# Kernel tuning notes

Measured on AMD Instinct MI355X. Metric: run time of the kernel, lower is better.

## Reference

```python
import jax, jax.numpy as jnp
import numpy as np

B, N, M, K = 4, 32768, 32768, 16
HID, DIM, G = 64, 32, 4
GN_EPS = 1e-5


def _conv1x1(x, w, b):
    # x: [B,C,N,K], w: [O,C], b: [O]  (1x1 Conv2d)
    return jnp.einsum('oc,bcnk->bonk', w, x) + b[None, :, None, None]


def _group_norm(x, w, b, groups):
    Bb, C, Nn, Kk = x.shape
    xg = x.reshape(Bb, groups, C // groups, Nn, Kk)
    mu = xg.mean(axis=(2, 3, 4), keepdims=True)
    var = xg.var(axis=(2, 3, 4), keepdims=True)
    xg = (xg - mu) * jax.lax.rsqrt(var + GN_EPS)
    x = xg.reshape(Bb, C, Nn, Kk)
    return x * w[None, :, None, None] + b[None, :, None, None]


def setup_inputs() -> dict:
    key = jax.random.key(0)
    ks = jax.random.split(key, 16)
    q_xyzs = jax.random.normal(ks[0], (B, 3, N), jnp.float32)
    k_xyzs = jax.random.normal(ks[1], (B, 3, M), jnp.float32)
    knn_idx = jax.random.randint(ks[2], (B, N, K), 0, M)
    mask = jax.random.randint(ks[3], (B, N, K), 0, 2).astype(bool)

    def w(k, o, c):
        return jax.random.normal(k, (o, c), jnp.float32) / np.sqrt(c)

    return {
        'q_xyzs': q_xyzs, 'k_xyzs': k_xyzs, 'knn_idx': knn_idx, 'mask': mask,
        'pre_w1': w(ks[4], HID, 4), 'pre_b1': jnp.zeros((HID,), jnp.float32),
        'pre_gn_w': jnp.ones((HID,), jnp.float32), 'pre_gn_b': jnp.zeros((HID,), jnp.float32),
        'pre_w2': w(ks[5], DIM, HID), 'pre_b2': jnp.zeros((DIM,), jnp.float32),
        'attn_w1': w(ks[6], HID, DIM), 'attn_b1': jnp.zeros((HID,), jnp.float32),
        'attn_gn_w': jnp.ones((HID,), jnp.float32), 'attn_gn_b': jnp.zeros((HID,), jnp.float32),
        'attn_w2': w(ks[7], DIM, HID), 'attn_b2': jnp.zeros((DIM,), jnp.float32),
    }


def reference(q_xyzs, k_xyzs, knn_idx, mask,
              pre_w1, pre_b1, pre_gn_w, pre_gn_b, pre_w2, pre_b2,
              attn_w1, attn_b1, attn_gn_w, attn_gn_b, attn_w2, attn_b2):
    # irregular gather: k_xyzs [B,3,M], knn_idx [B,N,K] -> knn_xyzs [B,3,N,K]
    knn_xyzs = jax.vmap(lambda pts, idx: pts[:, idx])(k_xyzs, knn_idx)
    diff = knn_xyzs - q_xyzs[..., None]                    # [B,3,N,K]
    dist = jnp.linalg.norm(diff, axis=1, keepdims=True)    # [B,1,N,K]
    direction = diff / jnp.maximum(dist, 1e-12)            # F.normalize(p=2, dim=1)
    local_pattern = jnp.concatenate([direction, dist], axis=1)  # [B,4,N,K]

    pe = _conv1x1(local_pattern, pre_w1, pre_b1)
    pe = jax.nn.relu(_group_norm(pe, pre_gn_w, pre_gn_b, G))
    pe = _conv1x1(pe, pre_w2, pre_b2)                      # [B,DIM,N,K]

    attn = _conv1x1(pe, attn_w1, attn_b1)
    attn = jax.nn.relu(_group_norm(attn, attn_gn_w, attn_gn_b, G))
    attn = _conv1x1(attn, attn_w2, attn_b2)                # [B,DIM,N,K]

    mask_value = -jnp.finfo(attn.dtype).max
    attn = jnp.where(mask[:, None], attn, mask_value)
    attn = jax.nn.softmax(attn, axis=-1)
    return (pe * attn).sum(axis=-1)                        # [B,DIM,N]
```

## Files before the change

### kernel.cpp

```cpp
#include <hip/hip_runtime.h>
#include <hip/hip_bf16.h>
#include <math.h>

#define NB 4
#define NN 32768
#define MM 32768
#define KK 16
#define HID 64
#define DIM 32
#define ENK (NN*KK)
#define EF  524288.0f
#define CNTG (16.0f*EF)
#define MASK_NEG (-60.0f)

#define WS_STATS1 0
#define WS_STATS2 64
#define WS_B1F    5312
#define WS_WA1H   5568
#define WS_BA1F   9664
#define WS_W2H    9920
#define WS_WA2H   10944
#define WS_W1H    11968
#define PE_BYTE_OFF 65536ull

typedef _Float16 h2v __attribute__((ext_vector_type(2)));
typedef _Float16 h8v __attribute__((ext_vector_type(8)));
typedef float f16v __attribute__((ext_vector_type(16)));

#if defined(__has_builtin)
#if __has_builtin(__builtin_amdgcn_fdot2)
#define USE_FDOT2 1
#endif
#endif
#ifndef USE_FDOT2
#define USE_FDOT2 0
#endif

__device__ __forceinline__ float dot2f(unsigned w, unsigned x, float acc) {
#if USE_FDOT2
  return __builtin_amdgcn_fdot2(__builtin_bit_cast(h2v, w),
                                __builtin_bit_cast(h2v, x), acc, false);
#else
  h2v a = __builtin_bit_cast(h2v, w);
  h2v b = __builtin_bit_cast(h2v, x);
  acc = fmaf((float)a[0], (float)b[0], acc);
  return fmaf((float)a[1], (float)b[1], acc);
#endif
}

__device__ __forceinline__ unsigned pkh(float a, float b) {
  return __builtin_bit_cast(unsigned, __builtin_amdgcn_cvt_pkrtz(a, b));
}

__device__ __forceinline__ f16v mfma16(uint4 a, uint4 b, f16v c) {
  return __builtin_amdgcn_mfma_f32_32x32x16_f16(
      __builtin_bit_cast(h8v, a), __builtin_bit_cast(h8v, b), c, 0, 0, 0);
}

template<int NV>
__device__ __forceinline__ void block_reduce_atomic(float* v, float* dst) {
  #pragma unroll
  for (int i = 0; i < NV; ++i) {
    float x = v[i];
    x += __shfl_down(x, 32);
    x += __shfl_down(x, 16);
    x += __shfl_down(x, 8);
    x += __shfl_down(x, 4);
    x += __shfl_down(x, 2);
    x += __shfl_down(x, 1);
    v[i] = x;
  }
  __shared__ float red[4][NV];
  const int lane = threadIdx.x & 63;
  const int wv = threadIdx.x >> 6;
  if (lane == 0) {
    #pragma unroll
    for (int i = 0; i < NV; ++i) red[wv][i] = v[i];
  }
  __syncthreads();
  if (threadIdx.x < NV) {
    float t = red[0][threadIdx.x] + red[1][threadIdx.x] +
              red[2][threadIdx.x] + red[3][threadIdx.x];
    atomicAdd(dst + threadIdx.x, t);
  }
}

__device__ __forceinline__ void compute_lp(const float* __restrict__ qb,
                                           const float* __restrict__ kb,
                                           int n, int idx,
                                           float& lp0, float& lp1, float& lp2, float& lp3) {
  float dx = kb[idx]        - qb[n];
  float dy = kb[MM + idx]   - qb[NN + n];
  float dz = kb[2*MM + idx] - qb[2*NN + n];
  float dist = sqrtf(fmaf(dx, dx, fmaf(dy, dy, dz*dz)));
  float inv = 1.0f / fmaxf(dist, 1e-12f);
  lp0 = dx * inv; lp1 = dy * inv; lp2 = dz * inv; lp3 = dist;
}

__global__ __launch_bounds__(256) void k_lpmom(
    const float* __restrict__ q_xyzs, const float* __restrict__ k_xyzs,
    const int* __restrict__ knn_idx,
    const float* __restrict__ w2, const float* __restrict__ wa2,
    float* __restrict__ ws)
{
  if (blockIdx.x == NB*256) {
    int t = threadIdx.x;
    unsigned* wsu = (unsigned*)ws;
    if (t < 32) {
      const float* src = w2 + t*64;
      unsigned* dst = wsu + WS_W2H + t*32;
      #pragma unroll
      for (int i = 0; i < 32; ++i) dst[i] = pkh(src[2*i], src[2*i+1]);
    } else if (t < 64) {
      int j = t - 32;
      const float* src = wa2 + j*64;
      unsigned* dst = wsu + WS_WA2H + j*32;
      #pragma unroll
      for (int i = 0; i < 32; ++i) dst[i] = pkh(src[2*i], src[2*i+1]);
    }
    return;
  }
  const int b   = blockIdx.x >> 8;
  const int blk = blockIdx.x & 255;
  const float* qb = q_xyzs + b*3*NN;
  const float* kb = k_xyzs + b*3*MM;
  const int* idxb = knn_idx + b*ENK;

  float a[14];
  #pragma unroll
  for (int i = 0; i < 14; ++i) a[i] = 0.f;

  for (int it = 0; it < 8; ++it) {
    int el = (blk*8 + it)*256 + threadIdx.x;
    int n = el >> 4;
    int idx = idxb[el];
    float lp0, lp1, lp2, lp3;
    compute_lp(qb, kb, n, idx, lp0, lp1, lp2, lp3);
    a[0] += lp0; a[1] += lp1; a[2] += lp2; a[3] += lp3;
    a[4] = fmaf(lp0, lp0, a[4]);  a[5] = fmaf(lp0, lp1, a[5]);
    a[6] = fmaf(lp0, lp2, a[6]);  a[7] = fmaf(lp0, lp3, a[7]);
    a[8] = fmaf(lp1, lp1, a[8]);  a[9] = fmaf(lp1, lp2, a[9]);
    a[10] = fmaf(lp1, lp3, a[10]); a[11] = fmaf(lp2, lp2, a[11]);
    a[12] = fmaf(lp2, lp3, a[12]); a[13] = fmaf(lp3, lp3, a[13]);
  }
  block_reduce_atomic<14>(a, ws + WS_STATS1 + b*16);
}

__global__ __launch_bounds__(64) void k_fold1(
    const float* __restrict__ w1, const float* __restrict__ b1,
    const float* __restrict__ gw, const float* __restrict__ gb,
    float* __restrict__ ws)
{
  int b = blockIdx.x, o = threadIdx.x;
  const float* st = ws + WS_STATS1 + b*16;
  float4 w = ((const float4*)w1)[o];
  float bb = b1[o];
  float dot = w.x*st[0] + w.y*st[1] + w.z*st[2] + w.w*st[3];
  float quad = w.x*w.x*st[4] + w.y*w.y*st[8] + w.z*w.z*st[11] + w.w*w.w*st[13]
    + 2.f*(w.x*w.y*st[5] + w.x*w.z*st[6] + w.x*w.w*st[7]
         + w.y*w.z*st[9] + w.y*w.w*st[10] + w.z*w.w*st[12]);
  float sum = dot + EF*bb;
  float ssq = quad + 2.f*bb*dot + EF*bb*bb;
  #pragma unroll
  for (int m = 1; m < 16; m <<= 1) {
    sum += __shfl_xor(sum, m);
    ssq += __shfl_xor(ssq, m);
  }
  float mu  = sum / CNTG;
  float var = ssq / CNTG - mu*mu;
  float sc  = rsqrtf(var + 1e-5f) * gw[o];
  unsigned* w1hd = (unsigned*)ws + WS_W1H + b*128;
  w1hd[o*2]   = pkh(w.x*sc, w.y*sc);
  w1hd[o*2+1] = pkh(w.z*sc, w.w*sc);
  (ws + WS_B1F)[b*64 + o] = (bb - mu)*sc + gb[o];
}

__global__ __launch_bounds__(256) void k_pe(
    const float* __restrict__ q_xyzs, const float* __restrict__ k_xyzs,
    const int* __restrict__ knn_idx, const float* __restrict__ b2,
    const float* __restrict__ ws, unsigned short* __restrict__ peh_ws)
{
  const int b  = blockIdx.x >> 8;
  const int l  = threadIdx.x & 63;
  const int wv = threadIdx.x >> 6;
  const int c  = l & 31;
  const int h  = l >> 5;
  const float* qb = q_xyzs + b*3*NN;
  const float* kb = k_xyzs + b*3*MM;

  const unsigned* w1h = (const unsigned*)ws + WS_W1H + b*128;
  const float* b1f = ws + WS_B1F + b*64;
  unsigned w01[32], w23[32];
  float bch[32];
  #pragma unroll
  for (int kc = 0; kc < 4; ++kc)
    #pragma unroll
    for (int jj = 0; jj < 8; ++jj) {
      int ch = kc*16 + h*8 + jj;
      w01[kc*8+jj] = w1h[ch*2];
      w23[kc*8+jj] = w1h[ch*2+1];
      bch[kc*8+jj] = b1f[ch];
    }
  const unsigned* w2h = (const unsigned*)ws + WS_W2H;
  uint4 A2[4];
  #pragma unroll
  for (int kc = 0; kc < 4; ++kc)
    A2[kc] = *(const uint4*)(w2h + c*32 + kc*8 + h*4);
  float bias2[16];
  #pragma unroll
  for (int r = 0; r < 16; ++r) bias2[r] = b2[(r&3) + 8*(r>>2) + 4*h];

  const int e0w = blockIdx.x*2048 + wv*512;

  int idx0 = knn_idx[e0w + c];
  float gxn = kb[idx0], gyn = kb[MM + idx0], gzn = kb[2*MM + idx0];

  #pragma unroll 1
  for (int tt = 0; tt < 16; ++tt) {
    const int e = e0w + tt*32 + c;
    int n = (e & (ENK-1)) >> 4;
    float gx = gxn, gy = gyn, gz = gzn;
    if (tt < 15) {
      int idn = knn_idx[e + 32];
      gxn = kb[idn]; gyn = kb[MM + idn]; gzn = kb[2*MM + idn];
    }
    float dx = gx - qb[n];
    float dy = gy - qb[NN + n];
    float dz = gz - qb[2*NN + n];
    float dist = sqrtf(fmaf(dx, dx, fmaf(dy, dy, dz*dz)));
    float inv = 1.0f / fmaxf(dist, 1e-12f);
    unsigned lp01 = pkh(dx*inv, dy*inv), lp23 = pkh(dz*inv, dist);

    uint4 Bf[4];
    #pragma unroll
    for (int kc = 0; kc < 4; ++kc) {
      unsigned bb[4];
      #pragma unroll
      for (int q = 0; q < 4; ++q) {
        int i0 = kc*8 + 2*q, i1 = i0 + 1;
        float xa = fmaxf(dot2f(w01[i0], lp01, dot2f(w23[i0], lp23, bch[i0])), 0.f);
        float xb = fmaxf(dot2f(w01[i1], lp01, dot2f(w23[i1], lp23, bch[i1])), 0.f);
        bb[q] = pkh(xa, xb);
      }
      Bf[kc] = make_uint4(bb[0], bb[1], bb[2], bb[3]);
    }

    f16v acc;
    #pragma unroll
    for (int r = 0; r < 16; ++r) acc[r] = bias2[r];
    #pragma unroll
    for (int kc = 0; kc < 4; ++kc) acc = mfma16(A2[kc], Bf[kc], acc);

    unsigned u[8], x[8];
    #pragma unroll
    for (int p = 0; p < 8; ++p) u[p] = pkh(acc[2*p], acc[2*p+1]);
    #pragma unroll
    for (int p = 0; p < 8; ++p) x[p] = __shfl_xor(u[p], 32);
    uint4 f0, f1;
    f0.x = h ? x[4] : u[0];  f0.y = h ? x[5] : u[1];
    f0.z = h ? u[4] : x[0];  f0.w = h ? u[5] : x[1];
    f1.x = h ? x[6] : u[2];  f1.y = h ? x[7] : u[3];
    f1.z = h ? u[6] : x[2];  f1.w = h ? u[7] : x[3];
    uint4* d = (uint4*)(peh_ws + (size_t)e*32 + h*16);
    d[0] = f0;
    d[1] = f1;
  }
}

__global__ __launch_bounds__(256) void k_pemom(
    const unsigned short* __restrict__ peh_ws, float* __restrict__ ws)
{
  const int b   = blockIdx.x >> 7;
  const int blk = blockIdx.x & 127;
  const int wv  = threadIdx.x >> 6;
  const int l   = threadIdx.x & 63;
  const int c   = l & 31;
  const int h   = l >> 5;

  const size_t ebase = (size_t)b*ENK + ((size_t)(blk*4 + wv))*1024;
  const unsigned short* pbase = peh_ws + ebase*32 + (size_t)h*8*32 + c;

  f16v acc;
  #pragma unroll
  for (int i = 0; i < 16; ++i) acc[i] = 0.f;
  float spe = 0.f;
  const unsigned ONE = pkh(1.f, 1.f);

  for (int t = 0; t < 64; ++t) {
    const unsigned short* p = pbase + (size_t)t*16*32;
    unsigned u0 = (unsigned)p[0*32]  | ((unsigned)p[1*32] << 16);
    unsigned u1 = (unsigned)p[2*32]  | ((unsigned)p[3*32] << 16);
    unsigned u2 = (unsigned)p[4*32]  | ((unsigned)p[5*32] << 16);
    unsigned u3 = (unsigned)p[6*32]  | ((unsigned)p[7*32] << 16);
    uint4 uu = make_uint4(u0, u1, u2, u3);
    h8v frag = __builtin_bit_cast(h8v, uu);
    acc = __builtin_amdgcn_mfma_f32_32x32x16_f16(frag, frag, acc, 0, 0, 0);
    spe = dot2f(u0, ONE, spe);
    spe = dot2f(u1, ONE, spe);
    spe = dot2f(u2, ONE, spe);
    spe = dot2f(u3, ONE, spe);
  }

  float* st2 = ws + WS_STATS2 + b*1056;
  spe += __shfl_down(spe, 32);
  if (l < 32) atomicAdd(st2 + c, spe);
  #pragma unroll
  for (int r = 0; r < 16; ++r) {
    int row = (r & 3) + 8*(r >> 2) + 4*h;
    atomicAdd(st2 + 32 + row*32 + c, acc[r]);
  }
}

__global__ __launch_bounds__(64) void k_fold2m(
    const float* __restrict__ wa1, const float* __restrict__ ba1,
    const float* __restrict__ gw2, const float* __restrict__ gb2,
    float* __restrict__ ws)
{
  int b = blockIdx.x, o = threadIdx.x;
  const float* st = ws + WS_STATS2 + b*1056;
  float w[32];
  const float4* wrow = (const float4*)wa1 + o*8;
  #pragma unroll
  for (int i = 0; i < 8; ++i) {
    float4 t = wrow[i];
    w[4*i] = t.x; w[4*i+1] = t.y; w[4*i+2] = t.z; w[4*i+3] = t.w;
  }
  float dot = 0.f;
  #pragma unroll
  for (int cc = 0; cc < 32; ++cc) dot = fmaf(w[cc], st[cc], dot);
  float quad = 0.f;
  #pragma unroll
  for (int rr = 0; rr < 32; ++rr) {
    const float* Mr = st + 32 + rr*32;
    float mr = 0.f;
    #pragma unroll
    for (int cc = 0; cc < 32; ++cc) mr = fmaf(Mr[cc], w[cc], mr);
    quad = fmaf(w[rr], mr, quad);
  }
  float bb = ba1[o];
  float sum = dot + EF*bb;
  float ssq = quad + 2.f*bb*dot + EF*bb*bb;
  #pragma unroll
  for (int m = 1; m < 16; m <<= 1) {
    sum += __shfl_xor(sum, m);
    ssq += __shfl_xor(ssq, m);
  }
  float mu  = sum / CNTG;
  float var = ssq / CNTG - mu*mu;
  float sc  = rsqrtf(var + 1e-5f) * gw2[o];
  unsigned* dst = (unsigned*)ws + WS_WA1H + (b*64 + o)*16;
  #pragma unroll
  for (int i2 = 0; i2 < 16; ++i2) dst[i2] = pkh(w[2*i2]*sc, w[2*i2+1]*sc);
  (ws + WS_BA1F)[b*64 + o] = (bb - mu)*sc + gb2[o];
}

__global__ __launch_bounds__(256) void k_out(
    const unsigned short* __restrict__ peh_ws, const int* __restrict__ mask,
    const float* __restrict__ ws, float* __restrict__ out)
{
  __shared__ float so[32][33];
  const int b  = blockIdx.x >> 10;
  const int l  = threadIdx.x & 63;
  const int wv = threadIdx.x >> 6;
  const int c  = l & 31;
  const int h  = l >> 5;

  const unsigned* wa1h = (const unsigned*)ws + WS_WA1H + b*1024;
  const unsigned* wa2h = (const unsigned*)ws + WS_WA2H;
  uint4 A1[2][2], A2w[4];
  #pragma unroll
  for (int t = 0; t < 2; ++t)
    #pragma unroll
    for (int kc = 0; kc < 2; ++kc)
      A1[t][kc] = *(const uint4*)(wa1h + (c + 32*t)*16 + kc*8 + h*4);
  #pragma unroll
  for (int kc2 = 0; kc2 < 4; ++kc2)
    A2w[kc2] = *(const uint4*)(wa2h + c*32 + kc2*8 + h*4);

  const float* ba1f = ws + WS_BA1F + b*64;
  float bias1[2][16];
  #pragma unroll
  for (int t = 0; t < 2; ++t)
    #pragma unroll
    for (int r = 0; r < 16; ++r)
      bias1[t][r] = ba1f[(r&3) + 8*(r>>2) + 4*h + 32*t];

  const int e0w = blockIdx.x*512 + wv*128;

  #pragma unroll
  for (int tt = 0; tt < 4; ++tt) {
    const int e0 = e0w + tt*32;
    const unsigned short* peb = peh_ws + (size_t)(e0 + c)*32 + h*8;
    uint4 peB0 = *(const uint4*)peb;
    uint4 peB1 = *(const uint4*)(peb + 16);

    f16v acc1a, acc1b;
    #pragma unroll
    for (int r = 0; r < 16; ++r) { acc1a[r] = bias1[0][r]; acc1b[r] = bias1[1][r]; }
    acc1a = mfma16(A1[0][0], peB0, acc1a);
    acc1a = mfma16(A1[0][1], peB1, acc1a);
    acc1b = mfma16(A1[1][0], peB0, acc1b);
    acc1b = mfma16(A1[1][1], peB1, acc1b);

    unsigned u0[8], u1[8], x0[8], x1[8];
    #pragma unroll
    for (int p = 0; p < 8; ++p) {
      u0[p] = pkh(fmaxf(acc1a[2*p], 0.f), fmaxf(acc1a[2*p+1], 0.f));
      u1[p] = pkh(fmaxf(acc1b[2*p], 0.f), fmaxf(acc1b[2*p+1], 0.f));
    }
    #pragma unroll
    for (int p = 0; p < 8; ++p) {
      x0[p] = __shfl_xor(u0[p], 32);
      x1[p] = __shfl_xor(u1[p], 32);
    }

    f16v acc2;
    #pragma unroll
    for (int r = 0; r < 16; ++r) acc2[r] = 0.f;
    #pragma unroll
    for (int kc2 = 0; kc2 < 4; ++kc2) {
      const int c1 = kc2 & 1;
      uint4 f;
      if ((kc2 >> 1) == 0) {
        f.x = h ? x0[4*c1+2] : u0[4*c1+0];
        f.y = h ? x0[4*c1+3] : u0[4*c1+1];
        f.z = h ? u0[4*c1+2] : x0[4*c1+0];
        f.w = h ? u0[4*c1+3] : x0[4*c1+1];
      } else {
        f.x = h ? x1[4*c1+2] : u1[4*c1+0];
        f.y = h ? x1[4*c1+3] : u1[4*c1+1];
        f.z = h ? u1[4*c1+2] : x1[4*c1+0];
        f.w = h ? u1[4*c1+3] : x1[4*c1+1];
      }
      acc2 = mfma16(f, A2w[kc2], acc2);
    }

    float v[16], pe_r[16];
    #pragma unroll
    for (int g = 0; g < 4; ++g) {
      int eb = 8*g + 4*h;
      int4 mm = *(const int4*)(mask + e0 + eb);
      v[4*g+0] = mm.x ? acc2[4*g+0] : MASK_NEG;
      v[4*g+1] = mm.y ? acc2[4*g+1] : MASK_NEG;
      v[4*g+2] = mm.z ? acc2[4*g+2] : MASK_NEG;
      v[4*g+3] = mm.w ? acc2[4*g+3] : MASK_NEG;
      #pragma unroll
      for (int i = 0; i < 4; ++i)
        pe_r[4*g+i] = (float)*(const _Float16*)(peh_ws + (size_t)(e0 + eb + i)*32 + c);
    }

    float sA = 0.f, wA = 0.f, sB = 0.f, wB = 0.f;
    #pragma unroll
    for (int r = 0; r < 8; ++r) {
      float pa = __expf(v[r]);
      float pb = __expf(v[r+8]);
      sA += pa; wA = fmaf(pa, pe_r[r],   wA);
      sB += pb; wB = fmaf(pb, pe_r[r+8], wB);
    }
    sA += __shfl_xor(sA, 32); wA += __shfl_xor(wA, 32);
    sB += __shfl_xor(sB, 32); wB += __shfl_xor(wB, 32);

    float num = h ? wB : wA;
    float den = h ? sB : sA;
    so[c][wv*8 + tt*2 + h] = __fdividef(num, den);
  }

  __syncthreads();
  const int n0 = (blockIdx.x & 1023) * 32;
  const int r = threadIdx.x >> 3, uu = threadIdx.x & 7;
  float4* dst = (float4*)(out + (size_t)b*(DIM*NN) + (size_t)r*NN + n0 + uu*4);
  dst[0] = *(float4*)&so[r][uu*4];
}

extern "C" void kernel_launch(void* const* d_in, const int* in_sizes, int n_in,
                              void* d_out, int out_size, void* d_ws, size_t ws_size,
                              hipStream_t stream) {
  (void)in_sizes; (void)n_in; (void)out_size; (void)ws_size;
  const float* q_xyzs   = (const float*)d_in[0];
  const float* k_xyzs   = (const float*)d_in[1];
  const int*   knn_idx  = (const int*)d_in[2];
  const int*   mask     = (const int*)d_in[3];
  const float* pre_w1   = (const float*)d_in[4];
  const float* pre_b1   = (const float*)d_in[5];
  const float* pre_gn_w = (const float*)d_in[6];
  const float* pre_gn_b = (const float*)d_in[7];
  const float* pre_w2   = (const float*)d_in[8];
  const float* pre_b2   = (const float*)d_in[9];
  const float* attn_w1  = (const float*)d_in[10];
  const float* attn_b1  = (const float*)d_in[11];
  const float* attn_gn_w= (const float*)d_in[12];
  const float* attn_gn_b= (const float*)d_in[13];
  const float* attn_w2  = (const float*)d_in[14];
  float* ws  = (float*)d_ws;
  float* out = (float*)d_out;
  unsigned short* peh_ws = (unsigned short*)((char*)d_ws + PE_BYTE_OFF);

  hipMemsetAsync(ws, 0, (64 + 4*1056)*sizeof(float), stream);
  k_lpmom <<<dim3(NB*256+1), 256, 0, stream>>>(q_xyzs, k_xyzs, knn_idx, pre_w2, attn_w2, ws);
  k_fold1 <<<dim3(NB),        64, 0, stream>>>(pre_w1, pre_b1, pre_gn_w, pre_gn_b, ws);
  k_pe    <<<dim3(NB*256),   256, 0, stream>>>(q_xyzs, k_xyzs, knn_idx, pre_b2, ws, peh_ws);
  k_pemom <<<dim3(NB*128),   256, 0, stream>>>(peh_ws, ws);
  k_fold2m<<<dim3(NB),        64, 0, stream>>>(attn_w1, attn_b1, attn_gn_w, attn_gn_b, ws);
  k_out   <<<dim3(NB*1024),  256, 0, stream>>>(peh_ws, mask, ws, out);
}
```

Before: 203.3 us.

## Store pe in MFMA-fragment order and permute weights to drop lane shuffles

Pe is now written in a per-32-edge tile layout that matches the MFMA accumulator and operand fragment order, so the producer kernel stores its accumulator registers directly instead of exchanging halves between lanes with shuffles. The attention weight matrices wa1 and wa2 are pre-permuted to the same ordering, which lets the output kernel feed the first MFMA's results straight into the second MFMA without cross-lane shuffles. The moments kernel and the per-element pe reads use new index arithmetic for this layout. The cost is more complex addressing, and the scattered 2-byte reads in the moments kernel and the output kernel may coalesce differently.

After: 225.0 us. 10.7% more time.

```diff
diff --git a/kernel.cpp b/kernel.cpp
--- a/kernel.cpp
+++ b/kernel.cpp
@@ -22,6 +22,7 @@
 #define WS_WA2H   10944
 #define WS_W1H    11968
 #define PE_BYTE_OFF 65536ull
+
 
 typedef _Float16 h2v __attribute__((ext_vector_type(2)));
 typedef _Float16 h8v __attribute__((ext_vector_type(8)));
@@ -111,12 +112,18 @@
       unsigned* dst = wsu + WS_W2H + t*32;
       #pragma unroll
       for (int i = 0; i < 32; ++i) dst[i] = pkh(src[2*i], src[2*i+1]);
-    } else if (t < 64) {
-      int j = t - 32;
+    } else if (t >= 64 && t < 128) {
+      int j  = (t - 64) & 31;
+      int hh = (t - 64) >> 5;
       const float* src = wa2 + j*64;
-      unsigned* dst = wsu + WS_WA2H + j*32;
+      unsigned* dst = wsu + WS_WA2H + (j*2 + hh)*16;
       #pragma unroll
-      for (int i = 0; i < 32; ++i) dst[i] = pkh(src[2*i], src[2*i+1]);
+      for (int kc2 = 0; kc2 < 4; ++kc2)
+        #pragma unroll
+        for (int pb = 0; pb < 4; ++pb) {
+          int base = 32*(kc2>>1) + 16*(kc2&1) + 8*(pb>>1) + 4*hh + 2*(pb&1);
+          dst[kc2*4 + pb] = pkh(src[base], src[base+1]);
+        }
     }
     return;
   }
@@ -217,7 +224,8 @@
 
   #pragma unroll 1
   for (int tt = 0; tt < 16; ++tt) {
-    const int e = e0w + tt*32 + c;
+    const int et = e0w + tt*32;
+    const int e = et + c;
     int n = (e & (ENK-1)) >> 4;
     float gx = gxn, gy = gyn, gz = gzn;
     if (tt < 15) {
@@ -251,19 +259,12 @@
     #pragma unroll
     for (int kc = 0; kc < 4; ++kc) acc = mfma16(A2[kc], Bf[kc], acc);
 
-    unsigned u[8], x[8];
+    unsigned u[8];
     #pragma unroll
     for (int p = 0; p < 8; ++p) u[p] = pkh(acc[2*p], acc[2*p+1]);
-    #pragma unroll
-    for (int p = 0; p < 8; ++p) x[p] = __shfl_xor(u[p], 32);
-    uint4 f0, f1;
-    f0.x = h ? x[4] : u[0];  f0.y = h ? x[5] : u[1];
-    f0.z = h ? u[4] : x[0];  f0.w = h ? u[5] : x[1];
-    f1.x = h ? x[6] : u[2];  f1.y = h ? x[7] : u[3];
-    f1.z = h ? u[6] : x[2];  f1.w = h ? u[7] : x[3];
-    uint4* d = (uint4*)(peh_ws + (size_t)e*32 + h*16);
-    d[0] = f0;
-    d[1] = f1;
+    uint4* d = (uint4*)(peh_ws + (size_t)et*32 + (size_t)(h*32 + c)*16);
+    d[0] = make_uint4(u[0], u[1], u[2], u[3]);
+    d[1] = make_uint4(u[4], u[5], u[6], u[7]);
   }
 }
 
@@ -277,8 +278,11 @@
   const int c   = l & 31;
   const int h   = l >> 5;
 
+  const int hc  = (c >> 2) & 1;
+  const int pc  = ((c >> 4) << 2) + (((c >> 3) & 1) << 1) + ((c >> 1) & 1);
+  const int offc = hc*512 + pc*2 + (c & 1);
+
   const size_t ebase = (size_t)b*ENK + ((size_t)(blk*4 + wv))*1024;
-  const unsigned short* pbase = peh_ws + ebase*32 + (size_t)h*8*32 + c;
 
   f16v acc;
   #pragma unroll
@@ -287,11 +291,12 @@
   const unsigned ONE = pkh(1.f, 1.f);
 
   for (int t = 0; t < 64; ++t) {
-    const unsigned short* p = pbase + (size_t)t*16*32;
-    unsigned u0 = (unsigned)p[0*32]  | ((unsigned)p[1*32] << 16);
-    unsigned u1 = (unsigned)p[2*32]  | ((unsigned)p[3*32] << 16);
-    unsigned u2 = (unsigned)p[4*32]  | ((unsigned)p[5*32] << 16);
-    unsigned u3 = (unsigned)p[6*32]  | ((unsigned)p[7*32] << 16);
+    const unsigned short* p = peh_ws + ebase*32 + (size_t)(t>>1)*1024
+                              + (t&1)*256 + h*128 + offc;
+    unsigned u0 = (unsigned)p[0]  | ((unsigned)p[16] << 16);
+    unsigned u1 = (unsigned)p[32] | ((unsigned)p[48] << 16);
+    unsigned u2 = (unsigned)p[64] | ((unsigned)p[80] << 16);
+    unsigned u3 = (unsigned)p[96] | ((unsigned)p[112] << 16);
     uint4 uu = make_uint4(u0, u1, u2, u3);
     h8v frag = __builtin_bit_cast(h8v, uu);
     acc = __builtin_amdgcn_mfma_f32_32x32x16_f16(frag, frag, acc, 0, 0, 0);
@@ -350,7 +355,14 @@
   float sc  = rsqrtf(var + 1e-5f) * gw2[o];
   unsigned* dst = (unsigned*)ws + WS_WA1H + (b*64 + o)*16;
   #pragma unroll
-  for (int i2 = 0; i2 < 16; ++i2) dst[i2] = pkh(w[2*i2]*sc, w[2*i2+1]*sc);
+  for (int kc = 0; kc < 2; ++kc)
+    #pragma unroll
+    for (int hh = 0; hh < 2; ++hh)
+      #pragma unroll
+      for (int p = 0; p < 4; ++p) {
+        int base = 16*kc + 8*(p>>1) + 4*hh + 2*(p&1);
+        dst[kc*8 + hh*4 + p] = pkh(w[base]*sc, w[base+1]*sc);
+      }
   (ws + WS_BA1F)[b*64 + o] = (bb - mu)*sc + gb2[o];
 }
 
@@ -375,7 +387,7 @@
       A1[t][kc] = *(const uint4*)(wa1h + (c + 32*t)*16 + kc*8 + h*4);
   #pragma unroll
   for (int kc2 = 0; kc2 < 4; ++kc2)
-    A2w[kc2] = *(const uint4*)(wa2h + c*32 + kc2*8 + h*4);
+    A2w[kc2] = *(const uint4*)(wa2h + (c*2 + h)*16 + kc2*4);
 
   const float* ba1f = ws + WS_BA1F + b*64;
   float bias1[2][16];
@@ -385,14 +397,18 @@
     for (int r = 0; r < 16; ++r)
       bias1[t][r] = ba1f[(r&3) + 8*(r>>2) + 4*h + 32*t];
 
+  const int hc  = (c >> 2) & 1;
+  const int pc  = ((c >> 4) << 2) + (((c >> 3) & 1) << 1) + ((c >> 1) & 1);
+  const int offc = hc*512 + pc*2 + (c & 1);
+
   const int e0w = blockIdx.x*512 + wv*128;
 
   #pragma unroll
   for (int tt = 0; tt < 4; ++tt) {
     const int e0 = e0w + tt*32;
-    const unsigned short* peb = peh_ws + (size_t)(e0 + c)*32 + h*8;
-    uint4 peB0 = *(const uint4*)peb;
-    uint4 peB1 = *(const uint4*)(peb + 16);
+    const uint4* peb = (const uint4*)(peh_ws + (size_t)e0*32 + (size_t)(h*32 + c)*16);
+    uint4 peB0 = peb[0];
+    uint4 peB1 = peb[1];
 
     f16v acc1a, acc1b;
     #pragma unroll
@@ -402,38 +418,20 @@
     acc1b = mfma16(A1[1][0], peB0, acc1b);
     acc1b = mfma16(A1[1][1], peB1, acc1b);
 
-    unsigned u0[8], u1[8], x0[8], x1[8];
+    unsigned u0[8], u1[8];
     #pragma unroll
     for (int p = 0; p < 8; ++p) {
       u0[p] = pkh(fmaxf(acc1a[2*p], 0.f), fmaxf(acc1a[2*p+1], 0.f));
       u1[p] = pkh(fmaxf(acc1b[2*p], 0.f), fmaxf(acc1b[2*p+1], 0.f));
     }
-    #pragma unroll
-    for (int p = 0; p < 8; ++p) {
-      x0[p] = __shfl_xor(u0[p], 32);
-      x1[p] = __shfl_xor(u1[p], 32);
-    }
 
     f16v acc2;
     #pragma unroll
     for (int r = 0; r < 16; ++r) acc2[r] = 0.f;
-    #pragma unroll
-    for (int kc2 = 0; kc2 < 4; ++kc2) {
-      const int c1 = kc2 & 1;
-      uint4 f;
-      if ((kc2 >> 1) == 0) {
-        f.x = h ? x0[4*c1+2] : u0[4*c1+0];
-        f.y = h ? x0[4*c1+3] : u0[4*c1+1];
-        f.z = h ? u0[4*c1+2] : x0[4*c1+0];
-        f.w = h ? u0[4*c1+3] : x0[4*c1+1];
-      } else {
-        f.x = h ? x1[4*c1+2] : u1[4*c1+0];
-        f.y = h ? x1[4*c1+3] : u1[4*c1+1];
-        f.z = h ? u1[4*c1+2] : x1[4*c1+0];
-        f.w = h ? u1[4*c1+3] : x1[4*c1+1];
-      }
-      acc2 = mfma16(f, A2w[kc2], acc2);
-    }
+    acc2 = mfma16(make_uint4(u0[0], u0[1], u0[2], u0[3]), A2w[0], acc2);
+    acc2 = mfma16(make_uint4(u0[4], u0[5], u0[6], u0[7]), A2w[1], acc2);
+    acc2 = mfma16(make_uint4(u1[0], u1[1], u1[2], u1[3]), A2w[2], acc2);
+    acc2 = mfma16(make_uint4(u1[4], u1[5], u1[6], u1[7]), A2w[3], acc2);
 
     float v[16], pe_r[16];
     #pragma unroll
@@ -446,7 +444,7 @@
       v[4*g+3] = mm.w ? acc2[4*g+3] : MASK_NEG;
       #pragma unroll
       for (int i = 0; i < 4; ++i)
-        pe_r[4*g+i] = (float)*(const _Float16*)(peh_ws + (size_t)(e0 + eb + i)*32 + c);
+        pe_r[4*g+i] = (float)*(const _Float16*)(peh_ws + (size_t)e0*32 + offc + (eb + i)*16);
     }
 
     float sA = 0.f, wA = 0.f, sB = 0.f, wB = 0.f;
```
